# Kernel optimization log

Hardware: AMD Instinct MI355X
Metric: run time of the kernel (lower is better)

Reference implementation:

```python
import jax, jax.numpy as jnp
import numpy as np

H, V, B, S = 2048, 32000, 16, 256

def setup_inputs() -> dict:
    key = jax.random.key(0)
    k1, k2, k3, k4 = jax.random.split(key, 4)
    # Parameters exactly as the torch __init__ builds them
    alpha_exp = jax.nn.softmax(jax.random.normal(k1, (H, H), dtype=jnp.float32), axis=1)   # transition probs [H,H]
    beta = jax.nn.log_softmax(jax.random.normal(k2, (H, V), dtype=jnp.float32), axis=1)    # emission log-probs [H,V]
    gamma = jax.nn.log_softmax(jax.random.normal(k3, (H,), dtype=jnp.float32), axis=0)     # initial-state logits [H]
    input_ids = jax.random.randint(k4, (B, S), 0, V)
    return {"input_ids": input_ids, "alpha_exp": alpha_exp, "beta": beta, "gamma": gamma}


def _hmm_forward(input_ids, alpha_exp, beta, gamma):
    # gamma stored as log-probs; forward re-softmaxes it (faithful to torch code)
    gamma_exp = jax.nn.softmax(gamma)                       # [H]
    ids = input_ids.T                                       # [S,B]
    mask = (ids != -1).astype(beta.dtype)                   # [S,B]; -1 = padding
    # input_probs[t,h,b] = beta[h, ids[t,b]] * mask
    ip = jnp.transpose(beta[:, ids], (1, 0, 2)) * mask[:, None, :]   # [S,H,B]
    ip_rev = ip[::-1]                                       # process t = S-1 .. 0

    def step(y, ipt):
        # log-domain backward recursion: y' = log(alpha_exp @ exp(y - ymax)) + ymax + emission
        ymax = jnp.max(y, axis=0, keepdims=True)            # [1,B]
        y = jnp.log(alpha_exp @ jnp.exp(y - ymax)) + ymax + ipt
        return y, y

    y0 = ip_rev[0]                                          # t = S-1: y starts at 0, += emission
    y_last, ys_rest = jax.lax.scan(step, y0, ip_rev[1:])
    ys = jnp.concatenate([y0[None], ys_rest], axis=0)       # [S,H,B], ys[i] is t = S-1-i

    ymax = jnp.max(y_last, axis=0)                          # [B]
    final = jnp.log(gamma_exp @ jnp.exp(y_last - ymax[None, :])) + ymax   # [B] per-seq loglik
    return ys, final


def reference(input_ids, alpha_exp, beta, gamma):
    return _hmm_forward(input_ids, alpha_exp, beta, gamma)
```

## Files before the change

kernel.cpp:

```cpp
#include <hip/hip_runtime.h>
#include <cstdint>
#include <cstddef>

#define Hh 2048
#define Vv 32000
#define Bb 16
#define Ss 256

typedef unsigned short ushort_t;
typedef unsigned int   uint_t;
typedef unsigned long long ull_t;

typedef __attribute__((ext_vector_type(8))) short short8;
typedef __attribute__((ext_vector_type(4))) float f32x4;

#define Z_OFF    0ull
#define Z_BYTES  ((size_t)2 * Bb * Hh * 2)
#define PM_OFF   (Z_OFF + Z_BYTES)
#define PM_BYTES ((size_t)8 * 256 * 32 * 2 * 4)
#define CNT_OFF  (PM_OFF + PM_BYTES)
#define CNT_BYTES ((size_t)8 * 256 * 4)
#define Y_OFF    (CNT_OFF + CNT_BYTES)
#define Y_BYTES  ((size_t)Bb * Hh * 4)
#define WS_NEED  (Y_OFF + Y_BYTES)

#define LD_REL(p)     __hip_atomic_load((p), __ATOMIC_RELAXED, __HIP_MEMORY_SCOPE_AGENT)
#define ST_REL(p, v)  __hip_atomic_store((p), (v), __ATOMIC_RELAXED, __HIP_MEMORY_SCOPE_AGENT)
#define ADD_REL(p)    __hip_atomic_fetch_add((p), 1u, __ATOMIC_RELAXED, __HIP_MEMORY_SCOPE_AGENT)

__device__ __forceinline__ float b2f_u(uint_t u) {
  union { uint_t u; float f; } x; x.u = u; return x.f;
}
__device__ __forceinline__ ushort_t f2b(float f) {
  union { float f; uint_t u; } x; x.f = f;
  uint_t u = x.u;
  return (ushort_t)((u + 0x7FFFu + ((u >> 16) & 1u)) >> 16);
}

__global__ __launch_bounds__(256, 1) void hmm_persist(
    const float* __restrict__ alpha,
    const float* __restrict__ beta,
    const int*  __restrict__ ids,
    ushort_t* __restrict__ Zbuf,
    float* __restrict__ pmax,
    uint_t* __restrict__ cnt,
    float* __restrict__ Y255,
    float* __restrict__ out)
{
  const int w    = blockIdx.x;
  const int g    = w & 7;
  const int wl   = w >> 3;
  const int c0   = g * 2;
  const int tid  = threadIdx.x;
  const int wv   = tid >> 6;
  const int lane = tid & 63;
  const int lrow = lane & 15;
  const int quad = lane >> 4;
  const int r0   = wl * 64 + wv * 16;

  __shared__ __align__(16) ushort_t zTf[2 * 2080];
  __shared__ float sclL[64];
  __shared__ float m01[2];
  __shared__ float red[4][2];
  __shared__ float ybuf[128];
  __shared__ float ipld[128];

  ull_t* Zb64 = (ull_t*)Zbuf;
  uint_t* Zb32 = (uint_t*)Zbuf;

  short8 afr[64];
  {
    const float* arow = alpha + (size_t)(r0 + lrow) * Hh + quad * 8;
    #pragma unroll
    for (int kt = 0; kt < 64; ++kt) {
      float4 f0 = *(const float4*)(arow + kt * 32);
      float4 f1 = *(const float4*)(arow + kt * 32 + 4);
      short8 fr;
      fr[0] = (short)f2b(f0.x); fr[1] = (short)f2b(f0.y);
      fr[2] = (short)f2b(f0.z); fr[3] = (short)f2b(f0.w);
      fr[4] = (short)f2b(f1.x); fr[5] = (short)f2b(f1.y);
      fr[6] = (short)f2b(f1.z); fr[7] = (short)f2b(f1.w);
      afr[kt] = fr;
    }
  }

  uint_t* mycnt = cnt + g * 256;
  const int myc = tid & 1;
  const int myr = wl * 64 + (tid >> 1);
  float ipreg = 0.f;

  {
    float yv = 0.f;
    if (tid < 128) {
      const int v = ids[(c0 + myc) * Ss + (Ss - 1)];
      yv = beta[(size_t)myr * Vv + v];
      ybuf[tid] = yv;
      out[(size_t)myr * Bb + (c0 + myc)] = yv;
    }
    __syncthreads();
    if (tid < 2) {
      float mm = -3.0e38f;
      for (int j = 0; j < 64; ++j) mm = fmaxf(mm, ybuf[2 * j + tid]);
      m01[tid] = mm;
      ST_REL(pmax + (size_t)(g * 256 + 0) * 64 + wl * 2 + tid, mm);
    }
    __syncthreads();
    if (tid < 64) {
      const int c = tid >> 5, rr0 = (tid & 31) * 2;
      const float mm = m01[c];
      uint_t lo = f2b(__expf(ybuf[rr0 * 2 + c] - mm));
      uint_t hi = f2b(__expf(ybuf[rr0 * 2 + 2 + c] - mm));
      ST_REL(Zb32 + (size_t)(c0 + c) * 1024 + (wl * 32 + (tid & 31)),
             lo | (hi << 16));
    }
    if (tid < 128) {
      const int v1 = ids[(c0 + myc) * Ss + (Ss - 2)];
      ipreg = beta[(size_t)myr * Vv + v1];
    }
    __syncthreads();
    if (tid == 0) ADD_REL(mycnt + 0);
  }

  const ushort_t* zbase = zTf + (lrow & 1) * 2080 + quad * 8;

  for (int k = 1; k < Ss; ++k) {
    const int zb = (k - 1) & 1;

    if (tid == 0) {
      while (LD_REL(mycnt + (k - 1)) != 32u) { }
    }
    __syncthreads();

    ull_t zr[4];
    {
      const size_t zB = (size_t)zb * 16 * 512;
      #pragma unroll
      for (int j = 0; j < 4; ++j) {
        const int idx = j * 256 + tid;
        const int c = idx >> 9;
        const int h4 = idx & 511;
        zr[j] = LD_REL(Zb64 + zB + (size_t)(c0 + c) * 512 + h4);
      }
    }

    if (tid < 64) {
      float pv = LD_REL(pmax + (size_t)(g * 256 + (k - 1)) * 64 + tid);
      float mr = pv;
      mr = fmaxf(mr, __shfl_xor(mr, 2));
      mr = fmaxf(mr, __shfl_xor(mr, 4));
      mr = fmaxf(mr, __shfl_xor(mr, 8));
      mr = fmaxf(mr, __shfl_xor(mr, 16));
      mr = fmaxf(mr, __shfl_xor(mr, 32));
      sclL[(tid & 1) * 32 + (tid >> 1)] = __expf(pv - mr);
      if (tid < 2) m01[tid] = mr;
    }
    __syncthreads();

    {
      #pragma unroll
      for (int j = 0; j < 4; ++j) {
        const int idx = j * 256 + tid;
        const int c = idx >> 9;
        const int h = (idx & 511) * 4;
        const float s = sclL[c * 32 + (h >> 6)];
        const ull_t u = zr[j];
        const uint_t lo = (uint_t)u, hi = (uint_t)(u >> 32);
        float z0 = b2f_u((lo & 0xFFFFu) << 16) * s;
        float z1 = b2f_u(lo & 0xFFFF0000u) * s;
        float z2 = b2f_u((hi & 0xFFFFu) << 16) * s;
        float z3 = b2f_u(hi & 0xFFFF0000u) * s;
        uint_t o0 = (uint_t)f2b(z0) | ((uint_t)f2b(z1) << 16);
        uint_t o1 = (uint_t)f2b(z2) | ((uint_t)f2b(z3) << 16);
        *(ull_t*)(zTf + c * 2080 + h) = (ull_t)o0 | ((ull_t)o1 << 32);
      }
      if (tid < 128) ipld[tid] = ipreg;
    }
    __syncthreads();

    if (k < Ss - 1 && tid < 128) {
      const int v = ids[(c0 + myc) * Ss + (Ss - 2 - k)];
      ipreg = beta[(size_t)myr * Vv + v];
    }

    f32x4 acc[8];
    {
      f32x4 zv = {0.f, 0.f, 0.f, 0.f};
      #pragma unroll
      for (int j = 0; j < 8; ++j) acc[j] = zv;
    }
    #pragma unroll
    for (int kt = 0; kt < 64; ++kt) {
      short8 bfr = *(const short8*)(zbase + kt * 32);
      acc[kt & 7] = __builtin_amdgcn_mfma_f32_16x16x32_bf16(afr[kt], bfr, acc[kt & 7], 0, 0, 0);
    }
    f32x4 sf = ((acc[0] + acc[1]) + (acc[2] + acc[3])) +
               ((acc[4] + acc[5]) + (acc[6] + acc[7]));

    const int  c   = lrow;
    const int  rb  = r0 + quad * 4;
    const int  lrr = wv * 16 + quad * 4;
    const bool act = (lrow < 2);
    const float mc = m01[lrow & 1];
    float yv4[4];
    float lm = -3.0e38f;
    if (act) {
      #pragma unroll
      for (int i = 0; i < 4; ++i) {
        float yv = __logf(sf[i]) + mc + ipld[(lrr + i) * 2 + c];
        yv4[i] = yv;
        lm = fmaxf(lm, yv);
      }
    }
    lm = fmaxf(lm, __shfl_xor(lm, 16));
    lm = fmaxf(lm, __shfl_xor(lm, 32));
    if (lane < 2) red[wv][lane] = lm;
    __syncthreads();

    float mch = 0.f;
    if (act) {
      mch = fmaxf(fmaxf(red[0][c], red[1][c]), fmaxf(red[2][c], red[3][c]));
      uint_t o0 = (uint_t)f2b(__expf(yv4[0] - mch)) | ((uint_t)f2b(__expf(yv4[1] - mch)) << 16);
      uint_t o1 = (uint_t)f2b(__expf(yv4[2] - mch)) | ((uint_t)f2b(__expf(yv4[3] - mch)) << 16);
      ST_REL(Zb64 + ((size_t)(k & 1) * 16 + (c0 + c)) * 512 + (rb >> 2),
             (ull_t)o0 | ((ull_t)o1 << 32));
    }
    if (tid < 2)
      ST_REL(pmax + (size_t)(g * 256 + k) * 64 + wl * 2 + tid, mch);
    __syncthreads();
    if (tid == 0) ADD_REL(mycnt + k);

    if (act) {
      #pragma unroll
      for (int i = 0; i < 4; ++i)
        out[(size_t)k * (Hh * Bb) + (size_t)(rb + i) * Bb + (c0 + c)] = yv4[i];
      if (k == Ss - 1) {
        float4 yo; yo.x = yv4[0]; yo.y = yv4[1]; yo.z = yv4[2]; yo.w = yv4[3];
        *(float4*)(Y255 + (size_t)(c0 + c) * Hh + rb) = yo;
      }
    }
  }
}

__global__ __launch_bounds__(256) void final_k(
    const float* __restrict__ gamma, const float* __restrict__ Y255,
    float* __restrict__ out)
{
  const int b = blockIdx.x;
  const int tid = threadIdx.x;
  __shared__ float sb[256];

  float ym = -3.0e38f;
  for (int h = tid; h < Hh; h += 256) ym = fmaxf(ym, Y255[(size_t)b * Hh + h]);
  sb[tid] = ym; __syncthreads();
  for (int off = 128; off; off >>= 1) {
    if (tid < off) sb[tid] = fmaxf(sb[tid], sb[tid + off]);
    __syncthreads();
  }
  ym = sb[0]; __syncthreads();

  float gm = -3.0e38f;
  for (int h = tid; h < Hh; h += 256) gm = fmaxf(gm, gamma[h]);
  sb[tid] = gm; __syncthreads();
  for (int off = 128; off; off >>= 1) {
    if (tid < off) sb[tid] = fmaxf(sb[tid], sb[tid + off]);
    __syncthreads();
  }
  gm = sb[0]; __syncthreads();

  float s1 = 0.f, s2 = 0.f;
  for (int h = tid; h < Hh; h += 256) {
    float gv = gamma[h] - gm;
    s1 += __expf(gv);
    s2 += __expf(gv + Y255[(size_t)b * Hh + h] - ym);
  }
  sb[tid] = s1; __syncthreads();
  for (int off = 128; off; off >>= 1) {
    if (tid < off) sb[tid] += sb[tid + off];
    __syncthreads();
  }
  s1 = sb[0]; __syncthreads();
  sb[tid] = s2; __syncthreads();
  for (int off = 128; off; off >>= 1) {
    if (tid < off) sb[tid] += sb[tid + off];
    __syncthreads();
  }
  s2 = sb[0];

  if (tid == 0)
    out[(size_t)Ss * Hh * Bb + b] = __logf(s2) - __logf(s1) + ym;
}

extern "C" void kernel_launch(void* const* d_in, const int* in_sizes, int n_in,
                              void* d_out, int out_size, void* d_ws, size_t ws_size,
                              hipStream_t stream) {
  (void)in_sizes; (void)n_in; (void)out_size;
  const int*   ids   = (const int*)d_in[0];
  const float* alpha = (const float*)d_in[1];
  const float* beta  = (const float*)d_in[2];
  const float* gamma = (const float*)d_in[3];
  float* out = (float*)d_out;
  char* ws = (char*)d_ws;

  if (ws_size < WS_NEED) return;

  ushort_t* Zbuf = (ushort_t*)(ws + Z_OFF);
  float*    pmax = (float*)(ws + PM_OFF);
  uint_t*   cnt  = (uint_t*)(ws + CNT_OFF);
  float*    Y255 = (float*)(ws + Y_OFF);

  hipMemsetAsync(cnt, 0, CNT_BYTES, stream);

  {
    const float* a_alpha = alpha;
    const float* a_beta  = beta;
    const int*   a_ids   = ids;
    ushort_t* a_z = Zbuf;  float* a_pm = pmax;  uint_t* a_cnt = cnt;
    float* a_y = Y255;     float* a_out = out;
    void* args[] = {(void*)&a_alpha, (void*)&a_beta, (void*)&a_ids, (void*)&a_z,
                    (void*)&a_pm, (void*)&a_cnt, (void*)&a_y, (void*)&a_out};
    hipError_t e = hipLaunchCooperativeKernel((const void*)hmm_persist,
                                              dim3(256), dim3(256), args, 0, stream);
    if (e != hipSuccess) {
      hipLaunchKernelGGL(hmm_persist, dim3(256), dim3(256), 0, stream,
                         alpha, beta, ids, Zbuf, pmax, cnt, Y255, out);
    }
  }

  hipLaunchKernelGGL(final_k, dim3(Bb), dim3(256), 0, stream, gamma, Y255, out);
}
```

Measured before the change: 1.574 ms.

## Replace counter barrier with sign-bit tagged data flags and lagged max normalization

Removes the per-step atomic counter and per-block partial-max exchange. Readiness is now signalled by the sign bit of each bf16 value in a triple-buffered Z array, so consumers spin directly on the data words. Normalization uses the previous step's running scale plus a max taken locally over the received Z. This eliminates a global counter round trip and several block barriers per timestep. The cost is per-word polling traffic and a looser normalization that could lose bf16 range or precision.

```diff
diff --git a/kernel.cpp b/kernel.cpp
--- a/kernel.cpp
+++ b/kernel.cpp
@@ -15,18 +15,17 @@
 typedef __attribute__((ext_vector_type(4))) float f32x4;
 
 #define Z_OFF    0ull
-#define Z_BYTES  ((size_t)2 * Bb * Hh * 2)
-#define PM_OFF   (Z_OFF + Z_BYTES)
-#define PM_BYTES ((size_t)8 * 256 * 32 * 2 * 4)
-#define CNT_OFF  (PM_OFF + PM_BYTES)
-#define CNT_BYTES ((size_t)8 * 256 * 4)
-#define Y_OFF    (CNT_OFF + CNT_BYTES)
+#define Z_SLOT   ((size_t)Bb * Hh * 2)
+#define Z_BYTES  ((size_t)3 * Z_SLOT)
+#define Y_OFF    (Z_OFF + Z_BYTES)
 #define Y_BYTES  ((size_t)Bb * Hh * 4)
 #define WS_NEED  (Y_OFF + Y_BYTES)
 
 #define LD_REL(p)     __hip_atomic_load((p), __ATOMIC_RELAXED, __HIP_MEMORY_SCOPE_AGENT)
 #define ST_REL(p, v)  __hip_atomic_store((p), (v), __ATOMIC_RELAXED, __HIP_MEMORY_SCOPE_AGENT)
-#define ADD_REL(p)    __hip_atomic_fetch_add((p), 1u, __ATOMIC_RELAXED, __HIP_MEMORY_SCOPE_AGENT)
+
+#define SGN64 0x8000800080008000ull
+#define MAG64 0x7FFF7FFF7FFF7FFFull
 
 __device__ __forceinline__ float b2f_u(uint_t u) {
   union { uint_t u; float f; } x; x.u = u; return x.f;
@@ -35,6 +34,12 @@
   union { float f; uint_t u; } x; x.f = f;
   uint_t u = x.u;
   return (ushort_t)((u + 0x7FFFu + ((u >> 16) & 1u)) >> 16);
+}
+__device__ __forceinline__ uint_t umaxu(uint_t a, uint_t b) { return a > b ? a : b; }
+__device__ __forceinline__ uint_t pkmax16(uint_t a, uint_t b) {
+  uint_t lo = umaxu(a & 0xFFFFu, b & 0xFFFFu);
+  uint_t hi = umaxu(a >> 16, b >> 16);
+  return lo | (hi << 16);
 }
 
 __global__ __launch_bounds__(256, 1) void hmm_persist(
@@ -42,8 +47,6 @@
     const float* __restrict__ beta,
     const int*  __restrict__ ids,
     ushort_t* __restrict__ Zbuf,
-    float* __restrict__ pmax,
-    uint_t* __restrict__ cnt,
     float* __restrict__ Y255,
     float* __restrict__ out)
 {
@@ -59,13 +62,11 @@
   const int r0   = wl * 64 + wv * 16;
 
   __shared__ __align__(16) ushort_t zTf[2 * 2080];
-  __shared__ float sclL[64];
-  __shared__ float m01[2];
-  __shared__ float red[4][2];
   __shared__ float ybuf[128];
   __shared__ float ipld[128];
-
-  ull_t* Zb64 = (ull_t*)Zbuf;
+  __shared__ uint_t redm[4];
+
+  ull_t*  Zb64 = (ull_t*)Zbuf;
   uint_t* Zb32 = (uint_t*)Zbuf;
 
   short8 afr[64];
@@ -84,7 +85,6 @@
     }
   }
 
-  uint_t* mycnt = cnt + g * 256;
   const int myc = tid & 1;
   const int myr = wl * 64 + (tid >> 1);
   float ipreg = 0.f;
@@ -98,18 +98,10 @@
       out[(size_t)myr * Bb + (c0 + myc)] = yv;
     }
     __syncthreads();
-    if (tid < 2) {
-      float mm = -3.0e38f;
-      for (int j = 0; j < 64; ++j) mm = fmaxf(mm, ybuf[2 * j + tid]);
-      m01[tid] = mm;
-      ST_REL(pmax + (size_t)(g * 256 + 0) * 64 + wl * 2 + tid, mm);
-    }
-    __syncthreads();
     if (tid < 64) {
       const int c = tid >> 5, rr0 = (tid & 31) * 2;
-      const float mm = m01[c];
-      uint_t lo = f2b(__expf(ybuf[rr0 * 2 + c] - mm));
-      uint_t hi = f2b(__expf(ybuf[rr0 * 2 + 2 + c] - mm));
+      uint_t lo = f2b(__expf(ybuf[rr0 * 2 + c]));
+      uint_t hi = f2b(__expf(ybuf[rr0 * 2 + 2 + c]));
       ST_REL(Zb32 + (size_t)(c0 + c) * 1024 + (wl * 32 + (tid & 31)),
              lo | (hi << 16));
     }
@@ -117,65 +109,61 @@
       const int v1 = ids[(c0 + myc) * Ss + (Ss - 2)];
       ipreg = beta[(size_t)myr * Vv + v1];
     }
-    __syncthreads();
-    if (tid == 0) ADD_REL(mycnt + 0);
-  }
-
+  }
+
+  float mprev = 0.f;
   const ushort_t* zbase = zTf + (lrow & 1) * 2080 + quad * 8;
 
   for (int k = 1; k < Ss; ++k) {
-    const int zb = (k - 1) & 1;
-
-    if (tid == 0) {
-      while (LD_REL(mycnt + (k - 1)) != 32u) { }
-    }
-    __syncthreads();
+    const int   physR = (3 - ((k - 1) % 3)) % 3;
+    const ull_t expS  = ((k - 1) & 1) ? SGN64 : 0ull;
 
     ull_t zr[4];
-    {
-      const size_t zB = (size_t)zb * 16 * 512;
-      #pragma unroll
-      for (int j = 0; j < 4; ++j) {
-        const int idx = j * 256 + tid;
-        const int c = idx >> 9;
-        const int h4 = idx & 511;
-        zr[j] = LD_REL(Zb64 + zB + (size_t)(c0 + c) * 512 + h4);
-      }
-    }
-
-    if (tid < 64) {
-      float pv = LD_REL(pmax + (size_t)(g * 256 + (k - 1)) * 64 + tid);
-      float mr = pv;
-      mr = fmaxf(mr, __shfl_xor(mr, 2));
-      mr = fmaxf(mr, __shfl_xor(mr, 4));
-      mr = fmaxf(mr, __shfl_xor(mr, 8));
-      mr = fmaxf(mr, __shfl_xor(mr, 16));
-      mr = fmaxf(mr, __shfl_xor(mr, 32));
-      sclL[(tid & 1) * 32 + (tid >> 1)] = __expf(pv - mr);
-      if (tid < 2) m01[tid] = mr;
-    }
-    __syncthreads();
-
-    {
-      #pragma unroll
-      for (int j = 0; j < 4; ++j) {
-        const int idx = j * 256 + tid;
-        const int c = idx >> 9;
-        const int h = (idx & 511) * 4;
-        const float s = sclL[c * 32 + (h >> 6)];
-        const ull_t u = zr[j];
-        const uint_t lo = (uint_t)u, hi = (uint_t)(u >> 32);
-        float z0 = b2f_u((lo & 0xFFFFu) << 16) * s;
-        float z1 = b2f_u(lo & 0xFFFF0000u) * s;
-        float z2 = b2f_u((hi & 0xFFFFu) << 16) * s;
-        float z3 = b2f_u(hi & 0xFFFF0000u) * s;
-        uint_t o0 = (uint_t)f2b(z0) | ((uint_t)f2b(z1) << 16);
-        uint_t o1 = (uint_t)f2b(z2) | ((uint_t)f2b(z3) << 16);
-        *(ull_t*)(zTf + c * 2080 + h) = (ull_t)o0 | ((ull_t)o1 << 32);
-      }
-      if (tid < 128) ipld[tid] = ipreg;
-    }
-    __syncthreads();
+    ull_t* zp[4];
+    #pragma unroll
+    for (int j = 0; j < 4; ++j) {
+      const int idx = j * 256 + tid;
+      const int c   = idx >> 9;
+      const int h4  = idx & 511;
+      zp[j] = Zb64 + (size_t)physR * (Bb * 512) + (size_t)(c0 + c) * 512 + h4;
+      zr[j] = LD_REL(zp[j]);
+    }
+    while (true) {
+      int bad = 0;
+      #pragma unroll
+      for (int j = 0; j < 4; ++j)
+        if ((zr[j] & SGN64) != expS) bad |= (1 << j);
+      if (!bad) break;
+      #pragma unroll
+      for (int j = 0; j < 4; ++j)
+        if (bad & (1 << j)) zr[j] = LD_REL(zp[j]);
+    }
+
+    uint_t mloc[2] = {0u, 0u};
+    #pragma unroll
+    for (int j = 0; j < 4; ++j) {
+      const ull_t v = zr[j] & MAG64;
+      const int idx = j * 256 + tid;
+      const int c   = idx >> 9;
+      const int h   = (idx & 511) * 4;
+      *(ull_t*)(zTf + c * 2080 + h) = v;
+      uint_t a = (uint_t)v, b = (uint_t)(v >> 32);
+      uint_t m2 = pkmax16(a, b);
+      mloc[j >> 1] = umaxu(mloc[j >> 1], umaxu(m2 & 0xFFFFu, m2 >> 16));
+    }
+    if (tid < 128) ipld[tid] = ipreg;
+
+    uint_t pk = mloc[0] | (mloc[1] << 16);
+    #pragma unroll
+    for (int d = 1; d < 64; d <<= 1)
+      pk = pkmax16(pk, __shfl_xor(pk, d));
+    if (lane == 0) redm[wv] = pk;
+    __syncthreads();
+
+    const uint_t rr  = pkmax16(pkmax16(redm[0], redm[1]),
+                               pkmax16(redm[2], redm[3]));
+    const uint_t mzb = (((lrow & 1) ? (rr >> 16) : (rr & 0xFFFFu)) << 16);
+    const float  lmax = __logf(b2f_u(mzb));
 
     if (k < Ss - 1 && tid < 128) {
       const int v = ids[(c0 + myc) * Ss + (Ss - 2 - k)];
@@ -200,36 +188,20 @@
     const int  rb  = r0 + quad * 4;
     const int  lrr = wv * 16 + quad * 4;
     const bool act = (lrow < 2);
-    const float mc = m01[lrow & 1];
-    float yv4[4];
-    float lm = -3.0e38f;
+    const int   physW = (3 - (k % 3)) % 3;
+    const ull_t orS   = (k & 1) ? SGN64 : 0ull;
+    const float mnew  = mprev + lmax;
     if (act) {
-      #pragma unroll
-      for (int i = 0; i < 4; ++i) {
-        float yv = __logf(sf[i]) + mc + ipld[(lrr + i) * 2 + c];
-        yv4[i] = yv;
-        lm = fmaxf(lm, yv);
-      }
-    }
-    lm = fmaxf(lm, __shfl_xor(lm, 16));
-    lm = fmaxf(lm, __shfl_xor(lm, 32));
-    if (lane < 2) red[wv][lane] = lm;
-    __syncthreads();
-
-    float mch = 0.f;
-    if (act) {
-      mch = fmaxf(fmaxf(red[0][c], red[1][c]), fmaxf(red[2][c], red[3][c]));
-      uint_t o0 = (uint_t)f2b(__expf(yv4[0] - mch)) | ((uint_t)f2b(__expf(yv4[1] - mch)) << 16);
-      uint_t o1 = (uint_t)f2b(__expf(yv4[2] - mch)) | ((uint_t)f2b(__expf(yv4[3] - mch)) << 16);
-      ST_REL(Zb64 + ((size_t)(k & 1) * 16 + (c0 + c)) * 512 + (rb >> 2),
-             (ull_t)o0 | ((ull_t)o1 << 32));
-    }
-    if (tid < 2)
-      ST_REL(pmax + (size_t)(g * 256 + k) * 64 + wl * 2 + tid, mch);
-    __syncthreads();
-    if (tid == 0) ADD_REL(mycnt + k);
-
-    if (act) {
+      float yv4[4];
+      #pragma unroll
+      for (int i = 0; i < 4; ++i)
+        yv4[i] = __logf(sf[i]) + mprev + ipld[(lrr + i) * 2 + c];
+      uint_t o0 = (uint_t)f2b(__expf(yv4[0] - mnew)) |
+                  ((uint_t)f2b(__expf(yv4[1] - mnew)) << 16);
+      uint_t o1 = (uint_t)f2b(__expf(yv4[2] - mnew)) |
+                  ((uint_t)f2b(__expf(yv4[3] - mnew)) << 16);
+      ST_REL(Zb64 + (size_t)physW * (Bb * 512) + (size_t)(c0 + c) * 512 + (rb >> 2),
+             ((ull_t)o0 | ((ull_t)o1 << 32)) | orS);
       #pragma unroll
       for (int i = 0; i < 4; ++i)
         out[(size_t)k * (Hh * Bb) + (size_t)(rb + i) * Bb + (c0 + c)] = yv4[i];
@@ -238,6 +210,8 @@
         *(float4*)(Y255 + (size_t)(c0 + c) * Hh + rb) = yo;
       }
     }
+    mprev = mnew;
+    __syncthreads();
   }
 }
 
@@ -304,25 +278,23 @@
   if (ws_size < WS_NEED) return;
 
   ushort_t* Zbuf = (ushort_t*)(ws + Z_OFF);
-  float*    pmax = (float*)(ws + PM_OFF);
-  uint_t*   cnt  = (uint_t*)(ws + CNT_OFF);
   float*    Y255 = (float*)(ws + Y_OFF);
 
-  hipMemsetAsync(cnt, 0, CNT_BYTES, stream);
+  hipMemsetAsync(ws + Z_OFF, 0x80, 2 * Z_SLOT, stream);
+  hipMemsetAsync(ws + Z_OFF + 2 * Z_SLOT, 0x00, Z_SLOT, stream);
 
   {
     const float* a_alpha = alpha;
     const float* a_beta  = beta;
     const int*   a_ids   = ids;
-    ushort_t* a_z = Zbuf;  float* a_pm = pmax;  uint_t* a_cnt = cnt;
-    float* a_y = Y255;     float* a_out = out;
-    void* args[] = {(void*)&a_alpha, (void*)&a_beta, (void*)&a_ids, (void*)&a_z,
-                    (void*)&a_pm, (void*)&a_cnt, (void*)&a_y, (void*)&a_out};
+    ushort_t* a_z = Zbuf;  float* a_y = Y255;  float* a_out = out;
+    void* args[] = {(void*)&a_alpha, (void*)&a_beta, (void*)&a_ids,
+                    (void*)&a_z, (void*)&a_y, (void*)&a_out};
     hipError_t e = hipLaunchCooperativeKernel((const void*)hmm_persist,
                                               dim3(256), dim3(256), args, 0, stream);
     if (e != hipSuccess) {
       hipLaunchKernelGGL(hmm_persist, dim3(256), dim3(256), 0, stream,
-                         alpha, beta, ids, Zbuf, pmax, cnt, Y255, out);
+                         alpha, beta, ids, Zbuf, Y255, out);
     }
   }
 
```

Result: slower. 1.607 ms (+2.1%).
